# Optimization experiments

Hardware: AMD Instinct MI355X
Metric: run time of the kernel (lower is better)

The kernel has to match this reference:

```python
import jax, jax.numpy as jnp
import numpy as np

N_NODES = 100000
N_EDGES = 1600000
D_IN = 128
D_OUT = 64
K_HOPS = 2


def setup_inputs() -> dict:
    key = jax.random.key(0)
    k1, k2, k3, k4, k5, k6, k7 = jax.random.split(key, 7)
    x = jax.random.normal(k1, (N_NODES, D_IN), dtype=jnp.float32)
    edge_index = jax.random.randint(k2, (2, N_EDGES), 0, N_NODES, dtype=jnp.int32)
    edge_weight = jax.random.uniform(k3, (N_EDGES,), dtype=jnp.float32)
    W1 = jax.random.normal(k4, (D_IN, D_IN), dtype=jnp.float32) * (1.0 / np.sqrt(D_IN))
    b1 = jax.random.normal(k5, (D_IN,), dtype=jnp.float32) * 0.01
    W2 = jax.random.normal(k6, (D_IN, D_OUT), dtype=jnp.float32) * (1.0 / np.sqrt(D_IN))
    b2 = jax.random.normal(k7, (D_OUT,), dtype=jnp.float32) * 0.01
    return {"x": x, "edge_index": edge_index, "edge_weight": edge_weight,
            "is_cluster": 0, "W1": W1, "b1": b1, "W2": W2, "b2": b2}


def reference(x, edge_index, edge_weight, is_cluster, W1, b1, W2, b2):
    # K-hop weighted sparse propagation: x <- scatter_add(x[src] * w, dst)
    src, dst = edge_index[0], edge_index[1]
    n = x.shape[0]
    for _ in range(K_HOPS):
        msgs = x[src] * edge_weight[:, None]          # [E, D] gather
        x = jax.ops.segment_sum(msgs, dst, num_segments=n)  # [N, D] scatter
    # transform (non-cluster path): lin1 -> relu -> lin2 -> log_softmax
    h = jax.nn.relu(x @ W1 + b1)
    logits = h @ W2 + b2
    return jax.nn.log_softmax(logits, axis=1)
```

## Files before the change

kernel.cpp:

```cpp
#include <hip/hip_runtime.h>
#include <cstdint>
#include <cstddef>

#define NN 100000
#define NE 1600000
#define D_IN 128
#define D_OUT 64
#define NB_BKT 391
#define BKT_CAP 4608
#define TILE 8192
#define CONVB 6250
#define PREPWB 24
#define GCURB 2

typedef __attribute__((ext_vector_type(8))) short bf16x8;
typedef __attribute__((ext_vector_type(4))) float f32x4;

__device__ __forceinline__ float bflo(unsigned u) {
    union { unsigned u; float f; } x; x.u = u << 16; return x.f;
}
__device__ __forceinline__ float bfhi(unsigned u) {
    union { unsigned u; float f; } x; x.u = u & 0xffff0000u; return x.f;
}
__device__ __forceinline__ unsigned f2b(float f) {
    union { float f; unsigned u; } x; x.f = f;
    unsigned u = x.u + 0x7fffu + ((x.u >> 16) & 1u);
    return u >> 16;
}

__device__ __forceinline__ void fma8(float* acc, uint4 v, float w) {
    acc[0] = fmaf(w, bflo(v.x), acc[0]);
    acc[1] = fmaf(w, bfhi(v.x), acc[1]);
    acc[2] = fmaf(w, bflo(v.y), acc[2]);
    acc[3] = fmaf(w, bfhi(v.y), acc[3]);
    acc[4] = fmaf(w, bflo(v.z), acc[4]);
    acc[5] = fmaf(w, bfhi(v.z), acc[5]);
    acc[6] = fmaf(w, bflo(v.w), acc[6]);
    acc[7] = fmaf(w, bfhi(v.w), acc[7]);
}

__global__ void __launch_bounds__(256) prep_all(
        const float4* __restrict__ x, uint4* __restrict__ xb,
        const float* __restrict__ W1, const float* __restrict__ W2,
        char* __restrict__ wt, int* __restrict__ gcur) {
    int b = blockIdx.x;
    int tid = threadIdx.x;
    if (b < CONVB) {
        int i = b * 256 + tid;
        float4 a = x[(size_t)i * 2], c = x[(size_t)i * 2 + 1];
        uint4 o;
        o.x = f2b(a.x) | (f2b(a.y) << 16);
        o.y = f2b(a.z) | (f2b(a.w) << 16);
        o.z = f2b(c.x) | (f2b(c.y) << 16);
        o.w = f2b(c.z) | (f2b(c.w) << 16);
        xb[i] = o;
    } else if (b < CONVB + PREPWB) {
        int t = (b - CONVB) * 256 + tid;
        if (t < 128 * 32) {
            int ch = t >> 5, kq = t & 31;
            unsigned lo = f2b(W1[(kq * 4 + 0) * 128 + ch]) | (f2b(W1[(kq * 4 + 1) * 128 + ch]) << 16);
            unsigned hi = f2b(W1[(kq * 4 + 2) * 128 + ch]) | (f2b(W1[(kq * 4 + 3) * 128 + ch]) << 16);
            *(uint2*)(wt + ch * 256 + kq * 8) = make_uint2(lo, hi);
        } else {
            int t2 = t - 128 * 32;
            int ch = t2 >> 5, kq = t2 & 31;
            unsigned lo = f2b(W2[(kq * 4 + 0) * 64 + ch]) | (f2b(W2[(kq * 4 + 1) * 64 + ch]) << 16);
            unsigned hi = f2b(W2[(kq * 4 + 2) * 64 + ch]) | (f2b(W2[(kq * 4 + 3) * 64 + ch]) << 16);
            *(uint2*)(wt + 32768 + ch * 256 + kq * 8) = make_uint2(lo, hi);
        }
    } else {
        int i = (b - CONVB - PREPWB) * 256 + tid;
        if (i < NB_BKT) gcur[i] = 0;
    }
}

__global__ void __launch_bounds__(256) fill_p1(
        const int* __restrict__ src, const int* __restrict__ dst,
        const float* __restrict__ w, int* __restrict__ gcur,
        int2* __restrict__ gbuf, int E) {
    __shared__ int cnt[NB_BKT];
    __shared__ int base[NB_BKT];
    int tid = threadIdx.x;
    int t0 = blockIdx.x * TILE;
    int t1 = min(t0 + TILE, E);
    for (int i = tid; i < NB_BKT; i += 256) cnt[i] = 0;
    __syncthreads();
    for (int e = t0 + tid; e < t1; e += 256)
        atomicAdd(&cnt[dst[e] >> 8], 1);
    __syncthreads();
    for (int i = tid; i < NB_BKT; i += 256) {
        int c = cnt[i];
        base[i] = c ? (i * BKT_CAP + atomicAdd(&gcur[i], c)) : 0;
        cnt[i] = 0;
    }
    __syncthreads();
    for (int e = t0 + tid; e < t1; e += 256) {
        int d = dst[e];
        int b = d >> 8;
        int r = atomicAdd(&cnt[b], 1);
        int pos = base[b] + r;
        if (pos < (b + 1) * BKT_CAP) {
            unsigned u = (unsigned)src[e] | ((unsigned)(d & 255) << 17);
            gbuf[pos] = make_int2((int)u, __float_as_int(w[e]));
        }
    }
}

__global__ void __launch_bounds__(256) fill_p2(
        const int2* __restrict__ gbuf, const int* __restrict__ gcur,
        int2* __restrict__ rownfo, unsigned* __restrict__ epk, int n) {
    __shared__ int2 sg[BKT_CAP];
    __shared__ unsigned se[BKT_CAP];
    __shared__ int cnt[256];
    __shared__ int lofs[256];
    __shared__ int pcnt[256];
    int tid = threadIdx.x;
    int bucket = blockIdx.x;
    int node0 = bucket << 8;
    int beg = bucket * BKT_CAP;
    int m = min(gcur[bucket], BKT_CAP);
    cnt[tid] = 0;
    pcnt[tid] = 0;
    __syncthreads();
    for (int i = tid; i < m; i += 256) {
        int2 p = gbuf[beg + i];
        sg[i] = p;
        atomicAdd(&cnt[(unsigned)p.x >> 17], 1);
    }
    __syncthreads();
    int v = cnt[tid];
    lofs[tid] = v;
    __syncthreads();
    for (int off = 1; off < 256; off <<= 1) {
        int t = (tid >= off) ? lofs[tid - off] : 0;
        __syncthreads();
        lofs[tid] += t;
        __syncthreads();
    }
    int myofs = lofs[tid] - v;
    __syncthreads();
    lofs[tid] = myofs;
    __syncthreads();
    for (int i = tid; i < m; i += 256) {
        int2 p = sg[i];
        unsigned u = (unsigned)p.x;
        int local = (int)(u >> 17);
        unsigned w15 = (unsigned)(__int_as_float(p.y) * 32767.0f + 0.5f);
        int r = atomicAdd(&pcnt[local], 1);
        se[lofs[local] + r] = (u & 0x1FFFFu) | (w15 << 17);
    }
    __syncthreads();
    for (int i = tid; i < m; i += 256) epk[beg + i] = se[i];
    int node = node0 + tid;
    if (node < n) rownfo[node] = make_int2(beg + myofs, beg + myofs + v);
}

__global__ void __launch_bounds__(256) prop_b(
        const uint4* __restrict__ xin, uint4* __restrict__ xout,
        const int2* __restrict__ rownfo, const unsigned* __restrict__ epk, int n) {
    int wid = (blockIdx.x * 256 + threadIdx.x) >> 6;
    if (wid >= n) return;
    int lane = threadIdx.x & 63;
    int q = lane >> 4, c = lane & 15;
    int2 be = rownfo[wid];
    int beg = be.x, end = be.y;
    const float ws = 1.0f / 32767.0f;
    float acc[8] = {0.f, 0.f, 0.f, 0.f, 0.f, 0.f, 0.f, 0.f};
    int e = beg + q;
    for (; e + 12 < end; e += 16) {
        unsigned p0 = epk[e];
        unsigned p1 = epk[e + 4];
        unsigned p2 = epk[e + 8];
        unsigned p3 = epk[e + 12];
        uint4 v0 = xin[(size_t)(p0 & 0x1FFFFu) * 16 + c];
        uint4 v1 = xin[(size_t)(p1 & 0x1FFFFu) * 16 + c];
        uint4 v2 = xin[(size_t)(p2 & 0x1FFFFu) * 16 + c];
        uint4 v3 = xin[(size_t)(p3 & 0x1FFFFu) * 16 + c];
        fma8(acc, v0, (float)(p0 >> 17) * ws);
        fma8(acc, v1, (float)(p1 >> 17) * ws);
        fma8(acc, v2, (float)(p2 >> 17) * ws);
        fma8(acc, v3, (float)(p3 >> 17) * ws);
    }
    if (e + 4 < end) {
        unsigned p0 = epk[e];
        unsigned p1 = epk[e + 4];
        uint4 v0 = xin[(size_t)(p0 & 0x1FFFFu) * 16 + c];
        uint4 v1 = xin[(size_t)(p1 & 0x1FFFFu) * 16 + c];
        fma8(acc, v0, (float)(p0 >> 17) * ws);
        fma8(acc, v1, (float)(p1 >> 17) * ws);
        e += 8;
    }
    if (e < end) {
        unsigned p0 = epk[e];
        uint4 v0 = xin[(size_t)(p0 & 0x1FFFFu) * 16 + c];
        fma8(acc, v0, (float)(p0 >> 17) * ws);
    }
    #pragma unroll
    for (int i = 0; i < 8; ++i) {
        acc[i] += __shfl_xor(acc[i], 16);
        acc[i] += __shfl_xor(acc[i], 32);
    }
    if (q == 0) {
        uint4 o;
        o.x = f2b(acc[0]) | (f2b(acc[1]) << 16);
        o.y = f2b(acc[2]) | (f2b(acc[3]) << 16);
        o.z = f2b(acc[4]) | (f2b(acc[5]) << 16);
        o.w = f2b(acc[6]) | (f2b(acc[7]) << 16);
        xout[(size_t)wid * 16 + c] = o;
    }
}

__global__ void __launch_bounds__(256) mlp_mfma(
        const unsigned short* __restrict__ y2b, const char* __restrict__ wt,
        const float* __restrict__ b1, const float* __restrict__ b2,
        float* __restrict__ out, int n) {
    __shared__ char lds[32768];
    int tid = threadIdx.x;
    int wave = tid >> 6, lane = tid & 63;
    int c = lane & 15, g = lane >> 4;
    int nb = blockIdx.x * 128 + wave * 32;
    char* ht = lds + wave * 8192;

    f32x4 acc[2][8];
    #pragma unroll
    for (int t = 0; t < 8; ++t) {
        float bv = b1[t * 16 + c];
        f32x4 v = {bv, bv, bv, bv};
        acc[0][t] = v; acc[1][t] = v;
    }
    #pragma unroll
    for (int ks = 0; ks < 4; ++ks) {
        bf16x8 a[2];
        #pragma unroll
        for (int r = 0; r < 2; ++r) {
            int row = nb + r * 16 + c;
            if (row >= n) row = n - 1;
            a[r] = *(const bf16x8*)(y2b + (size_t)row * 128 + ks * 32 + g * 8);
        }
        #pragma unroll
        for (int t = 0; t < 8; ++t) {
            int ch = t * 16 + c;
            bf16x8 b = *(const bf16x8*)(wt + ch * 256 + ks * 64 + g * 16);
            acc[0][t] = __builtin_amdgcn_mfma_f32_16x16x32_bf16(a[0], b, acc[0][t], 0, 0, 0);
            acc[1][t] = __builtin_amdgcn_mfma_f32_16x16x32_bf16(a[1], b, acc[1][t], 0, 0, 0);
        }
    }
    #pragma unroll
    for (int r = 0; r < 2; ++r) {
        #pragma unroll
        for (int t = 0; t < 8; ++t) {
            int ch = t * 16 + c;
            unsigned lo = f2b(fmaxf(acc[r][t][0], 0.f)) | (f2b(fmaxf(acc[r][t][1], 0.f)) << 16);
            unsigned hi = f2b(fmaxf(acc[r][t][2], 0.f)) | (f2b(fmaxf(acc[r][t][3], 0.f)) << 16);
            *(uint2*)(ht + ch * 64 + (r * 16 + g * 4) * 2) = make_uint2(lo, hi);
        }
    }
    __syncthreads();

    f32x4 g2[4][2];
    #pragma unroll
    for (int T = 0; T < 4; ++T) {
        float4 bb = *(const float4*)(b2 + T * 16 + g * 4);
        f32x4 v = {bb.x, bb.y, bb.z, bb.w};
        g2[T][0] = v; g2[T][1] = v;
    }
    #pragma unroll
    for (int ks = 0; ks < 4; ++ks) {
        bf16x8 aw[4];
        #pragma unroll
        for (int T = 0; T < 4; ++T) {
            int oc = T * 16 + c;
            aw[T] = *(const bf16x8*)(wt + 32768 + oc * 256 + ks * 64 + g * 16);
        }
        bf16x8 hb[2];
        #pragma unroll
        for (int p = 0; p < 2; ++p) {
            #pragma unroll
            for (int j = 0; j < 8; ++j) {
                int k = ks * 32 + g * 8 + j;
                hb[p][j] = *(const short*)(ht + k * 64 + (p * 16 + c) * 2);
            }
        }
        #pragma unroll
        for (int T = 0; T < 4; ++T) {
            #pragma unroll
            for (int p = 0; p < 2; ++p)
                g2[T][p] = __builtin_amdgcn_mfma_f32_16x16x32_bf16(aw[T], hb[p], g2[T][p], 0, 0, 0);
        }
    }

    #pragma unroll
    for (int p = 0; p < 2; ++p) {
        int node = nb + p * 16 + c;
        float m = -1e30f;
        #pragma unroll
        for (int T = 0; T < 4; ++T)
            #pragma unroll
            for (int j = 0; j < 4; ++j) m = fmaxf(m, g2[T][p][j]);
        m = fmaxf(m, __shfl_xor(m, 16));
        m = fmaxf(m, __shfl_xor(m, 32));
        float s = 0.f;
        #pragma unroll
        for (int T = 0; T < 4; ++T)
            #pragma unroll
            for (int j = 0; j < 4; ++j) s += __expf(g2[T][p][j] - m);
        s += __shfl_xor(s, 16);
        s += __shfl_xor(s, 32);
        float lse = m + __logf(s);
        if (node < n) {
            #pragma unroll
            for (int T = 0; T < 4; ++T) {
                float4 o = make_float4(g2[T][p][0] - lse, g2[T][p][1] - lse,
                                       g2[T][p][2] - lse, g2[T][p][3] - lse);
                *(float4*)(out + (size_t)node * 64 + T * 16 + g * 4) = o;
            }
        }
    }
}

extern "C" void kernel_launch(void* const* d_in, const int* in_sizes, int n_in,
                              void* d_out, int out_size, void* d_ws, size_t ws_size,
                              hipStream_t stream) {
    const float* x  = (const float*)d_in[0];
    const int*   ei = (const int*)  d_in[1];
    const float* w  = (const float*)d_in[2];
    const float* W1 = (const float*)d_in[4];
    const float* b1 = (const float*)d_in[5];
    const float* W2 = (const float*)d_in[6];
    const float* b2 = (const float*)d_in[7];
    float* out = (float*)d_out;

    const int n = NN, E = NE;
    const int* src = ei;
    const int* dst = ei + E;

    char* ws = (char*)d_ws;
    size_t off = 0;
    auto alloc = [&](size_t bytes) {
        char* p = ws + off;
        off += (bytes + 15) & ~(size_t)15;
        return p;
    };
    int*      gcur   = (int*)     alloc((size_t)NB_BKT * 4);
    int2*     rownfo = (int2*)    alloc((size_t)NN * 8);
    unsigned* epk    = (unsigned*)alloc((size_t)NB_BKT * BKT_CAP * 4);
    uint4*    xb     = (uint4*)   alloc((size_t)NN * D_IN * 2);
    uint4*    y1b    = (uint4*)   alloc((size_t)NN * D_IN * 2);
    uint4*    y2b    = (uint4*)   alloc((size_t)NN * D_IN * 2);
    char*     wt     = (char*)    alloc(49152);
    int2*     gbuf   = (int2*)y2b;

    prep_all<<<CONVB + PREPWB + GCURB, 256, 0, stream>>>(
        (const float4*)x, xb, W1, W2, wt, gcur);

    int ntile = (E + TILE - 1) / TILE;
    fill_p1<<<ntile, 256, 0, stream>>>(src, dst, w, gcur, gbuf, E);
    fill_p2<<<NB_BKT, 256, 0, stream>>>(gbuf, gcur, rownfo, epk, n);

    int pblocks = (n * 64 + 255) / 256;
    prop_b<<<pblocks, 256, 0, stream>>>(xb,  y1b, rownfo, epk, n);
    prop_b<<<pblocks, 256, 0, stream>>>(y1b, y2b, rownfo, epk, n);

    mlp_mfma<<<(n + 127) / 128, 256, 0, stream>>>((const unsigned short*)y2b, wt,
                                                  b1, b2, out, n);
}
```

Baseline: 248.9 us.

## Stage bucketed edges in LDS and write compact packed records coalesced

The first fill pass now sorts each tile's edges by bucket in shared memory, using a prefix scan over bucket counts, and then writes them out in contiguous runs per bucket through a binary search over bucket offsets. This replaces scattered 8-byte int2 writes with coalesced writes. Each edge is stored as a 4-byte packed src+quantized weight word plus a 1-byte local node id, and weight quantization moves from the second pass into the first. Block size rises to 512 and LDS use grows to about 45KB, which may reduce occupancy in exchange for cheaper global traffic in fill_p1 and fill_p2.

```diff
diff --git a/kernel.cpp b/kernel.cpp
--- a/kernel.cpp
+++ b/kernel.cpp
@@ -74,42 +74,74 @@
     }
 }
 
-__global__ void __launch_bounds__(256) fill_p1(
+__global__ void __launch_bounds__(512) fill_p1(
         const int* __restrict__ src, const int* __restrict__ dst,
         const float* __restrict__ w, int* __restrict__ gcur,
-        int2* __restrict__ gbuf, int E) {
+        unsigned* __restrict__ ebu, unsigned char* __restrict__ ebl, int E) {
+    __shared__ unsigned su[TILE];
+    __shared__ unsigned char sl[TILE];
     __shared__ int cnt[NB_BKT];
+    __shared__ int lofs[NB_BKT + 1];
     __shared__ int base[NB_BKT];
+    __shared__ int scan[512];
     int tid = threadIdx.x;
     int t0 = blockIdx.x * TILE;
     int t1 = min(t0 + TILE, E);
-    for (int i = tid; i < NB_BKT; i += 256) cnt[i] = 0;
-    __syncthreads();
-    for (int e = t0 + tid; e < t1; e += 256)
+    int m = t1 - t0;
+    for (int i = tid; i < NB_BKT; i += 512) cnt[i] = 0;
+    __syncthreads();
+    for (int e = t0 + tid; e < t1; e += 512)
         atomicAdd(&cnt[dst[e] >> 8], 1);
     __syncthreads();
-    for (int i = tid; i < NB_BKT; i += 256) {
-        int c = cnt[i];
-        base[i] = c ? (i * BKT_CAP + atomicAdd(&gcur[i], c)) : 0;
-        cnt[i] = 0;
-    }
-    __syncthreads();
-    for (int e = t0 + tid; e < t1; e += 256) {
+    int v = (tid < NB_BKT) ? cnt[tid] : 0;
+    scan[tid] = v;
+    __syncthreads();
+    for (int off = 1; off < 512; off <<= 1) {
+        int t = (tid >= off) ? scan[tid - off] : 0;
+        __syncthreads();
+        scan[tid] += t;
+        __syncthreads();
+    }
+    if (tid < NB_BKT) {
+        lofs[tid] = scan[tid] - v;
+        base[tid] = v ? atomicAdd(&gcur[tid], v) : 0;
+        cnt[tid] = 0;
+    }
+    if (tid == 0) lofs[NB_BKT] = m;
+    __syncthreads();
+    for (int e = t0 + tid; e < t1; e += 512) {
         int d = dst[e];
         int b = d >> 8;
+        unsigned w15 = (unsigned)(w[e] * 32767.0f + 0.5f);
         int r = atomicAdd(&cnt[b], 1);
-        int pos = base[b] + r;
-        if (pos < (b + 1) * BKT_CAP) {
-            unsigned u = (unsigned)src[e] | ((unsigned)(d & 255) << 17);
-            gbuf[pos] = make_int2((int)u, __float_as_int(w[e]));
+        int p = lofs[b] + r;
+        su[p] = (unsigned)src[e] | (w15 << 17);
+        sl[p] = (unsigned char)(d & 255);
+    }
+    __syncthreads();
+    for (int j = tid; j < m; j += 512) {
+        int lo = 0, hi = NB_BKT - 1;
+        #pragma unroll
+        for (int it = 0; it < 9; ++it) {
+            int mid = (lo + hi + 1) >> 1;
+            if (lofs[mid] <= j) lo = mid; else hi = mid - 1;
+        }
+        int b = lo;
+        int pos = base[b] + (j - lofs[b]);
+        if (pos < BKT_CAP) {
+            size_t g = (size_t)b * BKT_CAP + pos;
+            ebu[g] = su[j];
+            ebl[g] = sl[j];
         }
     }
 }
 
 __global__ void __launch_bounds__(256) fill_p2(
-        const int2* __restrict__ gbuf, const int* __restrict__ gcur,
-        int2* __restrict__ rownfo, unsigned* __restrict__ epk, int n) {
-    __shared__ int2 sg[BKT_CAP];
+        const unsigned* __restrict__ ebu, const unsigned char* __restrict__ ebl,
+        const int* __restrict__ gcur, int2* __restrict__ rownfo,
+        unsigned* __restrict__ epk, int n) {
+    __shared__ unsigned su[BKT_CAP];
+    __shared__ unsigned char slc[BKT_CAP];
     __shared__ unsigned se[BKT_CAP];
     __shared__ int cnt[256];
     __shared__ int lofs[256];
@@ -123,9 +155,10 @@
     pcnt[tid] = 0;
     __syncthreads();
     for (int i = tid; i < m; i += 256) {
-        int2 p = gbuf[beg + i];
-        sg[i] = p;
-        atomicAdd(&cnt[(unsigned)p.x >> 17], 1);
+        su[i] = ebu[beg + i];
+        int l = ebl[beg + i];
+        slc[i] = (unsigned char)l;
+        atomicAdd(&cnt[l], 1);
     }
     __syncthreads();
     int v = cnt[tid];
@@ -142,12 +175,9 @@
     lofs[tid] = myofs;
     __syncthreads();
     for (int i = tid; i < m; i += 256) {
-        int2 p = sg[i];
-        unsigned u = (unsigned)p.x;
-        int local = (int)(u >> 17);
-        unsigned w15 = (unsigned)(__int_as_float(p.y) * 32767.0f + 0.5f);
+        int local = slc[i];
         int r = atomicAdd(&pcnt[local], 1);
-        se[lofs[local] + r] = (u & 0x1FFFFu) | (w15 << 17);
+        se[lofs[local] + r] = su[i];
     }
     __syncthreads();
     for (int i = tid; i < m; i += 256) epk[beg + i] = se[i];
@@ -348,14 +378,15 @@
     uint4*    y1b    = (uint4*)   alloc((size_t)NN * D_IN * 2);
     uint4*    y2b    = (uint4*)   alloc((size_t)NN * D_IN * 2);
     char*     wt     = (char*)    alloc(49152);
-    int2*     gbuf   = (int2*)y2b;
+    unsigned*      ebu = (unsigned*)y2b;
+    unsigned char* ebl = (unsigned char*)y2b + (size_t)NB_BKT * BKT_CAP * 4;
 
     prep_all<<<CONVB + PREPWB + GCURB, 256, 0, stream>>>(
         (const float4*)x, xb, W1, W2, wt, gcur);
 
     int ntile = (E + TILE - 1) / TILE;
-    fill_p1<<<ntile, 256, 0, stream>>>(src, dst, w, gcur, gbuf, E);
-    fill_p2<<<NB_BKT, 256, 0, stream>>>(gbuf, gcur, rownfo, epk, n);
+    fill_p1<<<ntile, 512, 0, stream>>>(src, dst, w, gcur, ebu, ebl, E);
+    fill_p2<<<NB_BKT, 256, 0, stream>>>(ebu, ebl, gcur, rownfo, epk, n);
 
     int pblocks = (n * 64 + 255) / 256;
     prop_b<<<pblocks, 256, 0, stream>>>(xb,  y1b, rownfo, epk, n);
```

After: 240.8 us. 1.03x faster.
